# Kernel tuning notes

Measured on AMD Instinct MI355X. Metric: run time of the kernel, lower is better.

Reference implementation:

```python
import jax, jax.numpy as jnp
import numpy as np

B, S, NI, H = 64, 200, 50000, 256

def setup_inputs() -> dict:
    key = jax.random.key(0)
    ks = jax.random.split(key, 10)
    # trailing-padded sequences: lengths in [S//2, S]
    lengths = jax.random.randint(ks[0], (B,), S // 2, S + 1)
    t = jnp.arange(S)
    valid = t[None, :] < lengths[:, None]
    items = jnp.where(valid, jax.random.randint(ks[1], (B, S), 1, NI), 0)
    actions = jnp.where(valid, jax.random.randint(ks[2], (B, S), 0, 2), 0)
    sc = 1.0 / np.sqrt(H)
    # W_ih of nn.LSTM is [4H, 2*NI]; store transposed [2*NI, 4H] so one-hot matmul == row gather
    WihT = jax.random.uniform(ks[3], (2 * NI, 4 * H), jnp.float32, -sc, sc)
    Whh = jax.random.uniform(ks[4], (4 * H, H), jnp.float32, -sc, sc)
    b_lstm = jax.random.uniform(ks[5], (4 * H,), jnp.float32, -sc, sc)  # b_ih + b_hh
    trans_emb = jax.random.normal(ks[6], (NI, H), jnp.float32) * 0.05
    trans_emb = trans_emb.at[0].set(0.0)  # padding_idx=0
    Wq = jax.random.normal(ks[7], (2, H), jnp.float32) * sc
    bq = jnp.zeros((2,), jnp.float32)
    return {"items": items, "actions": actions, "WihT": WihT, "Whh": Whh,
            "b_lstm": b_lstm, "trans_emb": trans_emb, "Wq": Wq, "bq": bq}

def reference(items, actions, WihT, Whh, b_lstm, trans_emb, Wq, bq):
    ni = trans_emb.shape[0]
    h_dim = Whh.shape[1]
    it = items[:, :-1]    # [B,T]
    ac = actions[:, :-1]  # [B,T]
    mask = (it != 0)      # [B,T]
    # cat(one_hot(items,NI), one_hot(actions,NI)) @ W_ih.T == gather of two rows of WihT
    x_proj = (WihT[it] + WihT[ni + ac]) * mask[..., None].astype(WihT.dtype)  # [B,T,4H]

    def step(carry, inp):
        h, c = carry
        xp, m = inp  # xp: [B,4H], m: [B] bool
        gates = xp + h @ Whh.T + b_lstm
        i, f, g, o = jnp.split(gates, 4, axis=-1)  # torch gate order: i,f,g,o
        i = jax.nn.sigmoid(i); f = jax.nn.sigmoid(f)
        g = jnp.tanh(g);       o = jax.nn.sigmoid(o)
        c_new = f * c + i * g
        h_new = o * jnp.tanh(c_new)
        m = m[:, None]
        c = jnp.where(m, c_new, c)   # packed seq: state frozen past length
        h = jnp.where(m, h_new, h)
        out = jnp.where(m, h_new, 0.0)  # pad_packed pads outputs with zeros
        return (h, c), out

    b = items.shape[0]
    h0 = jnp.zeros((b, h_dim), WihT.dtype)
    (_, _), outs = jax.lax.scan(step, (h0, h0), (jnp.swapaxes(x_proj, 0, 1), mask.T))
    states = jnp.swapaxes(outs, 0, 1)  # [B,T,H]

    q_it = items[:, 1:]
    emb = trans_emb.at[0].set(0.0)[q_it]          # padding_idx=0 -> zero row
    query = (emb * states) @ Wq.T + bq            # [B,T,2]
    valid = (q_it != 0)
    targets = jnp.where(valid, actions[:, 1:], 0)
    logp = jax.nn.log_softmax(query, axis=-1)
    nll = -jnp.take_along_axis(logp, targets[..., None], axis=-1)[..., 0]
    vf = valid.astype(nll.dtype)
    # masked mean == F.cross_entropy over gathered (rows, cols) logits
    loss = jnp.sum(nll * vf) / jnp.sum(vf)
    return loss
```

## Files before the change

kernel.cpp:

```cpp
#include <hip/hip_runtime.h>
#include <stdint.h>

#define NITEMS 50000
#define SEQ    200
#define TMAX   199


template<int CTRL>
__device__ __forceinline__ float dpp_add(float x) {
    int r = __builtin_amdgcn_update_dpp(0, __float_as_int(x), CTRL, 0xF, 0xF, true);
    return x + __int_as_float(r);
}

__global__ __launch_bounds__(512, 2)
void lstm_main(const int* __restrict__ items, const int* __restrict__ actions,
               const float* __restrict__ WihT, const float* __restrict__ Whh,
               const float* __restrict__ b_lstm, const float* __restrict__ trans_emb,
               const float* __restrict__ Wq, const float* __restrict__ bq,
               int* flags, float* h_buf, float* accum)
{
    const int bid  = blockIdx.x;
    const int g    = (bid & 7) + 8 * ((bid >> 3) >> 2);
    const int q    = (bid >> 3) & 3;
    const int tid  = threadIdx.x;
    const int lane = tid & 63;
    const int wv   = tid >> 6;
    const int rg   = tid >> 4;
    const int kc   = tid & 15;

    __shared__ float xp_lds[2][256];
    __shared__ float gate_lds[256];
    __shared__ float b_lds[256];
    __shared__ float emb_lds[2][256];
    __shared__ float wq_lds[2][256];
    __shared__ float bq_lds[2];
    __shared__ int   items_s[SEQ];
    __shared__ int   act_s[SEQ];
    __shared__ int   len_sh;

    for (int i = tid; i < SEQ; i += 512) {
        items_s[i] = items[g * SEQ + i];
        act_s[i]   = actions[g * SEQ + i];
    }
    if (tid < 256) {
        b_lds[tid] = b_lstm[(tid >> 6) * 256 + q * 64 + (tid & 63)];
    } else {
        const int k = tid - 256;
        wq_lds[0][k] = Wq[k];
        wq_lds[1][k] = Wq[256 + k];
    }
    if (tid == 0) { bq_lds[0] = bq[0]; bq_lds[1] = bq[1]; }
    __syncthreads();
    if (tid == 0) {
        int L = 0;
        while (L < SEQ && items_s[L] != 0) ++L;
        len_sh = L;
    }
    __syncthreads();
    const int len = len_sh;
    const int L   = min(len, TMAX);

    float wgt[8][16];
    #pragma unroll
    for (int r = 0; r < 8; ++r) {
        const int r_blk = rg * 8 + r;
        const int j = (r_blk >> 6) * 256 + q * 64 + (r_blk & 63);
        const float4* wp = (const float4*)(Whh + (size_t)j * 256 + kc * 16);
        #pragma unroll
        for (int m = 0; m < 4; ++m) {
            float4 v = wp[m];
            wgt[r][4*m+0] = v.x; wgt[r][4*m+1] = v.y;
            wgt[r][4*m+2] = v.z; wgt[r][4*m+3] = v.w;
        }
    }

    if (wv == 0) {
        const int it = items_s[0], ac = act_s[0];
        const int c = lane >> 4, off = (lane & 15) * 4;
        float4 va = *(const float4*)(WihT + (size_t)it * 1024 + c * 256 + q * 64 + off);
        float4 vb = *(const float4*)(WihT + (size_t)(NITEMS + ac) * 1024 + c * 256 + q * 64 + off);
        *(float4*)&xp_lds[0][c * 64 + off] =
            make_float4(va.x+vb.x, va.y+vb.y, va.z+vb.z, va.w+vb.w);
    }
    if (q == 0 && wv == 2) {
        const int qe = items_s[1];
        float4 e = make_float4(0.f,0.f,0.f,0.f);
        if (qe != 0) e = *(const float4*)(trans_emb + (size_t)qe * 256 + 4 * lane);
        *(float4*)&emb_lds[0][4 * lane] = e;
    }
    __syncthreads();

    float c_cell = 0.f;
    float nll_acc = 0.f, cnt_acc = 0.f;
    float hreg[16];
    #pragma unroll
    for (int m = 0; m < 16; ++m) hreg[m] = 0.f;

    int*   myflags = flags + g * 32;
    float* hb      = h_buf + (size_t)g * 512;

    for (int t = 0; t < L; ++t) {
        if (t > 0) {
            if (tid < 4 && tid != q) {
                int guard = 0;
                while (__hip_atomic_load(&myflags[tid], __ATOMIC_ACQUIRE,
                                         __HIP_MEMORY_SCOPE_AGENT) < t) {
                    __builtin_amdgcn_s_sleep(1);
                    if (++guard > (1 << 16)) break;
                }
            }
            __syncthreads();
            unsigned long long* hp = (unsigned long long*)(hb + (t & 1) * 256 + kc * 16);
            #pragma unroll
            for (int m = 0; m < 8; ++m) {
                unsigned long long u = __hip_atomic_load(&hp[m], __ATOMIC_RELAXED,
                                                         __HIP_MEMORY_SCOPE_AGENT);
                union { unsigned long long u; float f[2]; } cv; cv.u = u;
                hreg[2*m]   = cv.f[0];
                hreg[2*m+1] = cv.f[1];
            }
        }

        const int tn = t + 1;
        float4 xa = make_float4(0,0,0,0), xb = make_float4(0,0,0,0);
        float4 ev = make_float4(0,0,0,0);
        float  he[4] = {0,0,0,0};
        if (wv == 1 && tn < L) {
            const int it = items_s[tn], ac = act_s[tn];
            const int c = lane >> 4, off = (lane & 15) * 4;
            xa = *(const float4*)(WihT + (size_t)it * 1024 + c * 256 + q * 64 + off);
            xb = *(const float4*)(WihT + (size_t)(NITEMS + ac) * 1024 + c * 256 + q * 64 + off);
        }
        if (q == 0 && wv == 2) {
            const int qe = items_s[tn];
            if (qe != 0) ev = *(const float4*)(trans_emb + (size_t)qe * 256 + 4 * lane);
            if (t >= 1) {
                unsigned long long* hp2 = (unsigned long long*)(hb + (t & 1) * 256 + 4 * lane);
                unsigned long long u0 = __hip_atomic_load(&hp2[0], __ATOMIC_RELAXED,
                                                          __HIP_MEMORY_SCOPE_AGENT);
                unsigned long long u1 = __hip_atomic_load(&hp2[1], __ATOMIC_RELAXED,
                                                          __HIP_MEMORY_SCOPE_AGENT);
                union { unsigned long long u; float f[2]; } c0, c1; c0.u = u0; c1.u = u1;
                he[0] = c0.f[0]; he[1] = c0.f[1]; he[2] = c1.f[0]; he[3] = c1.f[1];
            }
        }

        float acc[8];
        #pragma unroll
        for (int r = 0; r < 8; ++r) acc[r] = 0.f;
        #pragma unroll
        for (int m = 0; m < 16; ++m) {
            #pragma unroll
            for (int r = 0; r < 8; ++r) acc[r] = fmaf(wgt[r][m], hreg[m], acc[r]);
        }
        #pragma unroll
        for (int r = 0; r < 8; ++r) {
            float v = acc[r];
            v = dpp_add<0x128>(v);
            v = dpp_add<0x124>(v);
            v = dpp_add<0x122>(v);
            v = dpp_add<0x121>(v);
            acc[r] = v;
        }
        if (kc == 0) {
            #pragma unroll
            for (int r = 0; r < 8; ++r) {
                const int r_blk = rg * 8 + r;
                gate_lds[r_blk] = acc[r] + xp_lds[t & 1][r_blk] + b_lds[r_blk];
            }
        }
        __syncthreads();

        if (tid < 64) {
            const int d = tid;
            float gi = gate_lds[d];
            float gf = gate_lds[64 + d];
            float gg = gate_lds[128 + d];
            float go = gate_lds[192 + d];
            float ii = 1.f / (1.f + __expf(-gi));
            float ff = 1.f / (1.f + __expf(-gf));
            float oo = 1.f / (1.f + __expf(-go));
            float gt = tanhf(gg);
            c_cell = ff * c_cell + ii * gt;
            float hn = oo * tanhf(c_cell);
            __hip_atomic_store(&hb[((t + 1) & 1) * 256 + q * 64 + d], hn,
                               __ATOMIC_RELAXED, __HIP_MEMORY_SCOPE_AGENT);
            if (d == 0)
                __hip_atomic_store(&myflags[q], t + 1,
                                   __ATOMIC_RELEASE, __HIP_MEMORY_SCOPE_AGENT);
        } else if (wv == 1) {
            if (tn < L) {
                const int c = lane >> 4, off = (lane & 15) * 4;
                *(float4*)&xp_lds[tn & 1][c * 64 + off] =
                    make_float4(xa.x+xb.x, xa.y+xb.y, xa.z+xb.z, xa.w+xb.w);
            }
        } else if (wv == 2 && q == 0) {
            if (t >= 1) {
                const float* eb = &emb_lds[(t - 1) & 1][0];
                float s0 = 0.f, s1 = 0.f;
                #pragma unroll
                for (int m = 0; m < 4; ++m) {
                    const int k = 4 * lane + m;
                    float p = eb[k] * he[m];
                    s0 = fmaf(p, wq_lds[0][k], s0);
                    s1 = fmaf(p, wq_lds[1][k], s1);
                }
                #pragma unroll
                for (int off2 = 32; off2; off2 >>= 1) {
                    s0 += __shfl_xor(s0, off2);
                    s1 += __shfl_xor(s1, off2);
                }
                if (lane == 0) {
                    const int tgt = act_s[t];
                    float z0 = s0 + bq_lds[0], z1 = s1 + bq_lds[1];
                    float mz = fmaxf(z0, z1);
                    float lse = mz + __logf(__expf(z0 - mz) + __expf(z1 - mz));
                    nll_acc += lse - (tgt ? z1 : z0);
                    cnt_acc += 1.f;
                }
            }
            *(float4*)&emb_lds[t & 1][4 * lane] = ev;
        }
        __syncthreads();
    }

    if (q == 0 && wv == 2) {
        if (items_s[L] != 0) {
            if (lane < 4) {
                int guard = 0;
                while (__hip_atomic_load(&myflags[lane], __ATOMIC_ACQUIRE,
                                         __HIP_MEMORY_SCOPE_AGENT) < L) {
                    __builtin_amdgcn_s_sleep(1);
                    if (++guard > (1 << 16)) break;
                }
            }
            unsigned long long* hp2 = (unsigned long long*)(hb + (L & 1) * 256 + 4 * lane);
            unsigned long long u0 = __hip_atomic_load(&hp2[0], __ATOMIC_RELAXED,
                                                      __HIP_MEMORY_SCOPE_AGENT);
            unsigned long long u1 = __hip_atomic_load(&hp2[1], __ATOMIC_RELAXED,
                                                      __HIP_MEMORY_SCOPE_AGENT);
            union { unsigned long long u; float f[2]; } c0, c1; c0.u = u0; c1.u = u1;
            float he2[4] = { c0.f[0], c0.f[1], c1.f[0], c1.f[1] };
            const float* eb = &emb_lds[(L - 1) & 1][0];
            float s0 = 0.f, s1 = 0.f;
            #pragma unroll
            for (int m = 0; m < 4; ++m) {
                const int k = 4 * lane + m;
                float p = eb[k] * he2[m];
                s0 = fmaf(p, wq_lds[0][k], s0);
                s1 = fmaf(p, wq_lds[1][k], s1);
            }
            #pragma unroll
            for (int off2 = 32; off2; off2 >>= 1) {
                s0 += __shfl_xor(s0, off2);
                s1 += __shfl_xor(s1, off2);
            }
            if (lane == 0) {
                const int tgt = act_s[L];
                float z0 = s0 + bq_lds[0], z1 = s1 + bq_lds[1];
                float mz = fmaxf(z0, z1);
                float lse = mz + __logf(__expf(z0 - mz) + __expf(z1 - mz));
                nll_acc += lse - (tgt ? z1 : z0);
                cnt_acc += 1.f;
            }
        }
        if (lane == 0) {
            atomicAdd(&accum[0], nll_acc);
            atomicAdd(&accum[1], cnt_acc);
        }
    }
}

__global__ void finalize_k(const float* __restrict__ accum, float* __restrict__ out) {
    out[0] = accum[0] / accum[1];
}

extern "C" void kernel_launch(void* const* d_in, const int* in_sizes, int n_in,
                              void* d_out, int out_size, void* d_ws, size_t ws_size,
                              hipStream_t stream)
{
    const int*   items     = (const int*)d_in[0];
    const int*   actions   = (const int*)d_in[1];
    const float* WihT      = (const float*)d_in[2];
    const float* Whh       = (const float*)d_in[3];
    const float* b_lstm    = (const float*)d_in[4];
    const float* trans_emb = (const float*)d_in[5];
    const float* Wq        = (const float*)d_in[6];
    const float* bq        = (const float*)d_in[7];

    char*  ws    = (char*)d_ws;
    int*   flags = (int*)ws;
    float* accum = (float*)(ws + 8192);
    float* h_buf = (float*)(ws + 12288);

    hipMemsetAsync(d_ws, 0, 12288 + 64 * 2 * 256 * 4, stream);

    lstm_main<<<dim3(256), dim3(512), 0, stream>>>(
        items, actions, WihT, Whh, b_lstm, trans_emb, Wq, bq, flags, h_buf, accum);
    finalize_k<<<dim3(1), dim3(1), 0, stream>>>(accum, (float*)d_out);
}
```

Baseline: 1.492 ms.

## Replace flag-based cross-block sync with tagged (step,value) pairs and fuse gate update

Each hidden value is now published as a 64-bit pair carrying the step number, so consumer threads poll the data itself instead of waiting on per-block flags and a block barrier. Whh rows are regrouped so each 16-lane group owns all four gates for two hidden units, which removes the gate LDS round-trip and one barrier per step. The input projection is prefetched two steps ahead with a triple buffer, and the per-step end barrier waits only on LDS. The trade-off is twice the global traffic for h, every thread spinning on global loads, and launch bounds relaxed to one block per SIMD group.

```diff
diff --git a/kernel.cpp b/kernel.cpp
--- a/kernel.cpp
+++ b/kernel.cpp
@@ -4,6 +4,8 @@
 #define NITEMS 50000
 #define SEQ    200
 #define TMAX   199
+
+typedef unsigned long long u64;
 
 
 template<int CTRL>
@@ -12,12 +14,22 @@
     return x + __int_as_float(r);
 }
 
-__global__ __launch_bounds__(512, 2)
+__device__ __forceinline__ u64 ld_pair(const u64* p) {
+    return __hip_atomic_load(p, __ATOMIC_RELAXED, __HIP_MEMORY_SCOPE_AGENT);
+}
+__device__ __forceinline__ void st_pair(u64* p, u64 v) {
+    __hip_atomic_store(p, v, __ATOMIC_RELAXED, __HIP_MEMORY_SCOPE_AGENT);
+}
+__device__ __forceinline__ void step_barrier() {
+    asm volatile("s_waitcnt lgkmcnt(0)\n\ts_barrier" ::: "memory");
+}
+
+__global__ __launch_bounds__(512, 1)
 void lstm_main(const int* __restrict__ items, const int* __restrict__ actions,
                const float* __restrict__ WihT, const float* __restrict__ Whh,
                const float* __restrict__ b_lstm, const float* __restrict__ trans_emb,
                const float* __restrict__ Wq, const float* __restrict__ bq,
-               int* flags, float* h_buf, float* accum)
+               u64* pairs, float* accum)
 {
     const int bid  = blockIdx.x;
     const int g    = (bid & 7) + 8 * ((bid >> 3) >> 2);
@@ -28,8 +40,7 @@
     const int rg   = tid >> 4;
     const int kc   = tid & 15;
 
-    __shared__ float xp_lds[2][256];
-    __shared__ float gate_lds[256];
+    __shared__ float xp_lds[3][256];
     __shared__ float b_lds[256];
     __shared__ float emb_lds[2][256];
     __shared__ float wq_lds[2][256];
@@ -50,30 +61,29 @@
         wq_lds[1][k] = Wq[256 + k];
     }
     if (tid == 0) { bq_lds[0] = bq[0]; bq_lds[1] = bq[1]; }
-    __syncthreads();
-    if (tid == 0) {
-        int L = 0;
-        while (L < SEQ && items_s[L] != 0) ++L;
-        len_sh = L;
-    }
-    __syncthreads();
-    const int len = len_sh;
-    const int L   = min(len, TMAX);
 
     float wgt[8][16];
     #pragma unroll
-    for (int r = 0; r < 8; ++r) {
-        const int r_blk = rg * 8 + r;
-        const int j = (r_blk >> 6) * 256 + q * 64 + (r_blk & 63);
-        const float4* wp = (const float4*)(Whh + (size_t)j * 256 + kc * 16);
-        #pragma unroll
-        for (int m = 0; m < 4; ++m) {
-            float4 v = wp[m];
-            wgt[r][4*m+0] = v.x; wgt[r][4*m+1] = v.y;
-            wgt[r][4*m+2] = v.z; wgt[r][4*m+3] = v.w;
-        }
-    }
-
+    for (int gt = 0; gt < 4; ++gt) {
+        #pragma unroll
+        for (int e = 0; e < 2; ++e) {
+            const int j = gt * 256 + q * 64 + 2 * rg + e;
+            const float4* wp = (const float4*)(Whh + (size_t)j * 256 + kc * 16);
+            #pragma unroll
+            for (int m2 = 0; m2 < 4; ++m2) {
+                float4 v = wp[m2];
+                wgt[gt*2+e][4*m2+0] = v.x; wgt[gt*2+e][4*m2+1] = v.y;
+                wgt[gt*2+e][4*m2+2] = v.z; wgt[gt*2+e][4*m2+3] = v.w;
+            }
+        }
+    }
+    __syncthreads();
+
+    if (tid == 0) {
+        int Lx = 0;
+        while (Lx < SEQ && items_s[Lx] != 0) ++Lx;
+        len_sh = Lx;
+    }
     if (wv == 0) {
         const int it = items_s[0], ac = act_s[0];
         const int c = lane >> 4, off = (lane & 15) * 4;
@@ -81,68 +91,57 @@
         float4 vb = *(const float4*)(WihT + (size_t)(NITEMS + ac) * 1024 + c * 256 + q * 64 + off);
         *(float4*)&xp_lds[0][c * 64 + off] =
             make_float4(va.x+vb.x, va.y+vb.y, va.z+vb.z, va.w+vb.w);
-    }
-    if (q == 0 && wv == 2) {
-        const int qe = items_s[1];
-        float4 e = make_float4(0.f,0.f,0.f,0.f);
-        if (qe != 0) e = *(const float4*)(trans_emb + (size_t)qe * 256 + 4 * lane);
-        *(float4*)&emb_lds[0][4 * lane] = e;
+    } else if (wv == 1) {
+        const int it = items_s[1], ac = act_s[1];
+        const int c = lane >> 4, off = (lane & 15) * 4;
+        float4 va = *(const float4*)(WihT + (size_t)it * 1024 + c * 256 + q * 64 + off);
+        float4 vb = *(const float4*)(WihT + (size_t)(NITEMS + ac) * 1024 + c * 256 + q * 64 + off);
+        *(float4*)&xp_lds[1][c * 64 + off] =
+            make_float4(va.x+vb.x, va.y+vb.y, va.z+vb.z, va.w+vb.w);
     }
     __syncthreads();
-
-    float c_cell = 0.f;
+    const int len = len_sh;
+    const int L   = min(len, TMAX);
+
+    float c0 = 0.f, c1 = 0.f;
     float nll_acc = 0.f, cnt_acc = 0.f;
     float hreg[16];
     #pragma unroll
     for (int m = 0; m < 16; ++m) hreg[m] = 0.f;
 
-    int*   myflags = flags + g * 32;
-    float* hb      = h_buf + (size_t)g * 512;
+    u64* gbuf = pairs + (size_t)g * 512;
 
     for (int t = 0; t < L; ++t) {
+        const int xs = t % 3;
         if (t > 0) {
-            if (tid < 4 && tid != q) {
-                int guard = 0;
-                while (__hip_atomic_load(&myflags[tid], __ATOMIC_ACQUIRE,
-                                         __HIP_MEMORY_SCOPE_AGENT) < t) {
-                    __builtin_amdgcn_s_sleep(1);
-                    if (++guard > (1 << 16)) break;
-                }
-            }
-            __syncthreads();
-            unsigned long long* hp = (unsigned long long*)(hb + (t & 1) * 256 + kc * 16);
-            #pragma unroll
-            for (int m = 0; m < 8; ++m) {
-                unsigned long long u = __hip_atomic_load(&hp[m], __ATOMIC_RELAXED,
-                                                         __HIP_MEMORY_SCOPE_AGENT);
-                union { unsigned long long u; float f[2]; } cv; cv.u = u;
-                hreg[2*m]   = cv.f[0];
-                hreg[2*m+1] = cv.f[1];
-            }
-        }
-
-        const int tn = t + 1;
+            const u64* src = gbuf + (t & 1) * 256 + kc * 16;
+            u64 v[16];
+            int guard = 0;
+            for (;;) {
+                #pragma unroll
+                for (int m = 0; m < 16; ++m) v[m] = ld_pair(src + m);
+                unsigned ok = 1u;
+                #pragma unroll
+                for (int m = 0; m < 16; ++m) ok &= (unsigned)((unsigned)v[m] == (unsigned)t);
+                if (ok || ++guard > (1 << 16)) break;
+            }
+            #pragma unroll
+            for (int m = 0; m < 16; ++m)
+                hreg[m] = __uint_as_float((unsigned)(v[m] >> 32));
+        }
+
+        const int tn2 = t + 2;
         float4 xa = make_float4(0,0,0,0), xb = make_float4(0,0,0,0);
         float4 ev = make_float4(0,0,0,0);
-        float  he[4] = {0,0,0,0};
-        if (wv == 1 && tn < L) {
-            const int it = items_s[tn], ac = act_s[tn];
+        if (wv == 1 && tn2 < L) {
+            const int it = items_s[tn2], ac = act_s[tn2];
             const int c = lane >> 4, off = (lane & 15) * 4;
             xa = *(const float4*)(WihT + (size_t)it * 1024 + c * 256 + q * 64 + off);
             xb = *(const float4*)(WihT + (size_t)(NITEMS + ac) * 1024 + c * 256 + q * 64 + off);
         }
         if (q == 0 && wv == 2) {
-            const int qe = items_s[tn];
+            const int qe = items_s[t + 1];
             if (qe != 0) ev = *(const float4*)(trans_emb + (size_t)qe * 256 + 4 * lane);
-            if (t >= 1) {
-                unsigned long long* hp2 = (unsigned long long*)(hb + (t & 1) * 256 + 4 * lane);
-                unsigned long long u0 = __hip_atomic_load(&hp2[0], __ATOMIC_RELAXED,
-                                                          __HIP_MEMORY_SCOPE_AGENT);
-                unsigned long long u1 = __hip_atomic_load(&hp2[1], __ATOMIC_RELAXED,
-                                                          __HIP_MEMORY_SCOPE_AGENT);
-                union { unsigned long long u; float f[2]; } c0, c1; c0.u = u0; c1.u = u1;
-                he[0] = c0.f[0]; he[1] = c0.f[1]; he[2] = c1.f[0]; he[3] = c1.f[1];
-            }
         }
 
         float acc[8];
@@ -162,46 +161,44 @@
             v = dpp_add<0x121>(v);
             acc[r] = v;
         }
+
         if (kc == 0) {
             #pragma unroll
-            for (int r = 0; r < 8; ++r) {
-                const int r_blk = rg * 8 + r;
-                gate_lds[r_blk] = acc[r] + xp_lds[t & 1][r_blk] + b_lds[r_blk];
-            }
-        }
-        __syncthreads();
-
-        if (tid < 64) {
-            const int d = tid;
-            float gi = gate_lds[d];
-            float gf = gate_lds[64 + d];
-            float gg = gate_lds[128 + d];
-            float go = gate_lds[192 + d];
-            float ii = 1.f / (1.f + __expf(-gi));
-            float ff = 1.f / (1.f + __expf(-gf));
-            float oo = 1.f / (1.f + __expf(-go));
-            float gt = tanhf(gg);
-            c_cell = ff * c_cell + ii * gt;
-            float hn = oo * tanhf(c_cell);
-            __hip_atomic_store(&hb[((t + 1) & 1) * 256 + q * 64 + d], hn,
-                               __ATOMIC_RELAXED, __HIP_MEMORY_SCOPE_AGENT);
-            if (d == 0)
-                __hip_atomic_store(&myflags[q], t + 1,
-                                   __ATOMIC_RELEASE, __HIP_MEMORY_SCOPE_AGENT);
-        } else if (wv == 1) {
-            if (tn < L) {
-                const int c = lane >> 4, off = (lane & 15) * 4;
-                *(float4*)&xp_lds[tn & 1][c * 64 + off] =
-                    make_float4(xa.x+xb.x, xa.y+xb.y, xa.z+xb.z, xa.w+xb.w);
-            }
-        } else if (wv == 2 && q == 0) {
+            for (int e = 0; e < 2; ++e) {
+                const int d = 2 * rg + e;
+                float gi = acc[0 + e] + xp_lds[xs][      d] + b_lds[      d];
+                float gf = acc[2 + e] + xp_lds[xs][ 64 + d] + b_lds[ 64 + d];
+                float gg = acc[4 + e] + xp_lds[xs][128 + d] + b_lds[128 + d];
+                float go = acc[6 + e] + xp_lds[xs][192 + d] + b_lds[192 + d];
+                float ii = 1.f / (1.f + __expf(-gi));
+                float ff = 1.f / (1.f + __expf(-gf));
+                float oo = 1.f / (1.f + __expf(-go));
+                float gv = tanhf(gg);
+                float cn = ff * (e ? c1 : c0) + ii * gv;
+                if (e) c1 = cn; else c0 = cn;
+                float hn = oo * tanhf(cn);
+                u64 pv = (u64)(unsigned)(t + 1) | ((u64)__float_as_uint(hn) << 32);
+                st_pair(gbuf + ((t + 1) & 1) * 256 + q * 64 + d, pv);
+            }
+        }
+
+        if (wv == 1 && tn2 < L) {
+            const int c = lane >> 4, off = (lane & 15) * 4;
+            *(float4*)&xp_lds[tn2 % 3][c * 64 + off] =
+                make_float4(xa.x+xb.x, xa.y+xb.y, xa.z+xb.z, xa.w+xb.w);
+        }
+        if (q == 0 && wv == 2) {
             if (t >= 1) {
+                const int b4 = lane >> 4;
+                const int k0 = 16 * (lane & 15) + 4 * b4;
                 const float* eb = &emb_lds[(t - 1) & 1][0];
                 float s0 = 0.f, s1 = 0.f;
                 #pragma unroll
                 for (int m = 0; m < 4; ++m) {
-                    const int k = 4 * lane + m;
-                    float p = eb[k] * he[m];
+                    float hv = (b4 == 0) ? hreg[m] : (b4 == 1) ? hreg[4 + m]
+                             : (b4 == 2) ? hreg[8 + m] : hreg[12 + m];
+                    const int k = k0 + m;
+                    float p = eb[k] * hv;
                     s0 = fmaf(p, wq_lds[0][k], s0);
                     s1 = fmaf(p, wq_lds[1][k], s1);
                 }
@@ -221,32 +218,31 @@
             }
             *(float4*)&emb_lds[t & 1][4 * lane] = ev;
         }
-        __syncthreads();
+
+        step_barrier();
     }
 
     if (q == 0 && wv == 2) {
         if (items_s[L] != 0) {
-            if (lane < 4) {
-                int guard = 0;
-                while (__hip_atomic_load(&myflags[lane], __ATOMIC_ACQUIRE,
-                                         __HIP_MEMORY_SCOPE_AGENT) < L) {
-                    __builtin_amdgcn_s_sleep(1);
-                    if (++guard > (1 << 16)) break;
-                }
-            }
-            unsigned long long* hp2 = (unsigned long long*)(hb + (L & 1) * 256 + 4 * lane);
-            unsigned long long u0 = __hip_atomic_load(&hp2[0], __ATOMIC_RELAXED,
-                                                      __HIP_MEMORY_SCOPE_AGENT);
-            unsigned long long u1 = __hip_atomic_load(&hp2[1], __ATOMIC_RELAXED,
-                                                      __HIP_MEMORY_SCOPE_AGENT);
-            union { unsigned long long u; float f[2]; } c0, c1; c0.u = u0; c1.u = u1;
-            float he2[4] = { c0.f[0], c0.f[1], c1.f[0], c1.f[1] };
+            const int b4 = lane >> 4;
+            const int k0 = 16 * (lane & 15) + 4 * b4;
+            const u64* s2 = gbuf + (L & 1) * 256 + k0;
+            u64 w[4];
+            int guard = 0;
+            for (;;) {
+                #pragma unroll
+                for (int m = 0; m < 4; ++m) w[m] = ld_pair(s2 + m);
+                unsigned ok = 1u;
+                #pragma unroll
+                for (int m = 0; m < 4; ++m) ok &= (unsigned)((unsigned)w[m] == (unsigned)L);
+                if (ok || ++guard > (1 << 16)) break;
+            }
             const float* eb = &emb_lds[(L - 1) & 1][0];
             float s0 = 0.f, s1 = 0.f;
             #pragma unroll
             for (int m = 0; m < 4; ++m) {
-                const int k = 4 * lane + m;
-                float p = eb[k] * he2[m];
+                const int k = k0 + m;
+                float p = eb[k] * __uint_as_float((unsigned)(w[m] >> 32));
                 s0 = fmaf(p, wq_lds[0][k], s0);
                 s1 = fmaf(p, wq_lds[1][k], s1);
             }
@@ -289,13 +285,12 @@
     const float* bq        = (const float*)d_in[7];
 
     char*  ws    = (char*)d_ws;
-    int*   flags = (int*)ws;
     float* accum = (float*)(ws + 8192);
-    float* h_buf = (float*)(ws + 12288);
-
-    hipMemsetAsync(d_ws, 0, 12288 + 64 * 2 * 256 * 4, stream);
+    u64*   pairs = (u64*)(ws + 16384);
+
+    hipMemsetAsync(d_ws, 0, 16384 + 64 * 2 * 256 * 8, stream);
 
     lstm_main<<<dim3(256), dim3(512), 0, stream>>>(
-        items, actions, WihT, Whh, b_lstm, trans_emb, Wq, bq, flags, h_buf, accum);
+        items, actions, WihT, Whh, b_lstm, trans_emb, Wq, bq, pairs, accum);
     finalize_k<<<dim3(1), dim3(1), 0, stream>>>(accum, (float*)d_out);
 }
```

After: 1.594 ms. 6.9% more time.
